# Optimization experiments

Hardware: AMD Instinct MI355X
Metric: run time of the kernel (lower is better)

## Reference

```python
import jax, jax.numpy as jnp
import numpy as np

BLOCK = 64      # sparse block size (power of 2, >= 16)
NB = 128        # number of blocks -> max_seqlen = 8192
LOCAL = 8       # causal local window, in blocks
GLOBAL = 1      # leading global blocks every query attends to
K = LOCAL + GLOBAL
SM_SCALE = 1.0 / np.sqrt(64.0)  # default sm_scale = 1/sqrt(head_dim)


def _build_layout():
    # Fixed-width equivalent of the CSR block layout: for query block i,
    # live key blocks are the GLOBAL leading blocks plus the LOCAL-wide
    # causal window ending at i. Entries outside [0, i] are masked invalid;
    # global entries that fall inside the local window are invalidated to
    # avoid double counting.
    rows = np.arange(NB)[:, None]
    loc = rows - np.arange(LOCAL - 1, -1, -1)[None, :]      # [NB, LOCAL], ascending, ends at i
    glb = np.tile(np.arange(GLOBAL)[None, :], (NB, 1))      # [NB, GLOBAL]
    loc_valid = loc >= 0
    glb_valid = glb < (rows - LOCAL + 1)                    # strictly below local window
    col = np.concatenate([glb, np.maximum(loc, 0)], axis=1)  # [NB, K]
    valid = np.concatenate([glb_valid, loc_valid], axis=1)   # [NB, K]
    return col.astype(np.int32), valid


def setup_inputs() -> dict:
    key = jax.random.key(0)
    kq, kk, kv = jax.random.split(key, 3)
    B, S, H, D = 2, NB * BLOCK, 16, 64
    q = jax.random.normal(kq, (B, S, H, D), jnp.float32)
    k = jax.random.normal(kk, (B, S, H, D), jnp.float32)
    v = jax.random.normal(kv, (B, S, H, D), jnp.float32)
    col, valid = _build_layout()
    return {"q": q, "k": k, "v": v,
            "col_idx": jnp.asarray(col), "col_valid": jnp.asarray(valid)}


def reference(q, k, v, col_idx, col_valid):
    # Block-sparse causal attention. Only key/value blocks listed in
    # col_idx (where col_valid) are touched; token-level causal mask is
    # applied inside the gathered blocks (diagonal blocks get intra-block
    # causal masking, matching the kernel's behavior).
    B, S, H, D = q.shape
    bs = BLOCK
    nb = S // bs
    qb = q.reshape(B, nb, bs, H, D)                       # [B, nb, bs, H, D]
    kb = k.reshape(B, nb, bs, H, D)[:, col_idx]           # [B, nb, K, bs, H, D]
    vb = v.reshape(B, nb, bs, H, D)[:, col_idx]
    scores = jnp.einsum('bimhd,bijnhd->bhimjn', qb, kb) * SM_SCALE  # [B,H,nb,bs,K,bs]
    qpos = jnp.arange(nb)[:, None] * bs + jnp.arange(bs)[None, :]          # [nb, bs]
    kpos = col_idx[:, :, None] * bs + jnp.arange(bs)[None, None, :]        # [nb, K, bs]
    mask = (kpos[:, None, :, :] <= qpos[:, :, None, None]) & col_valid[:, None, :, None]
    neg = jnp.finfo(scores.dtype).min
    scores = jnp.where(mask[None, None], scores, neg)
    shp = scores.shape
    p = jax.nn.softmax(scores.reshape(shp[0], shp[1], shp[2], shp[3], -1), axis=-1).reshape(shp)
    out = jnp.einsum('bhimjn,bijnhd->bimhd', p, vb)       # [B, nb, bs, H, D]
    return out.reshape(B, S, H, D)
```

## Files before the change

kernel.cpp:

```cpp
#include <hip/hip_runtime.h>
#include <hip/hip_bf16.h>

#define NBQ     128
#define NLOCAL  8
#define NH      16
#define NBATCH  2
#define DIM     64
#define SEQ     (NBQ * 64)
#define QK_SCALE 0.1803368801111204f

typedef __attribute__((ext_vector_type(8))) short bf16x8;
typedef __attribute__((ext_vector_type(4))) short short4v;
typedef __attribute__((ext_vector_type(4))) float f32x4;
typedef __attribute__((ext_vector_type(2))) unsigned int u32x2;

__device__ inline short f2b(float x) {
    unsigned int u = __float_as_uint(x);
    return (short)((u + 0x8000u) >> 16);
}
__device__ inline unsigned int pack2(unsigned int lo_rnd, unsigned int hi_rnd) {
    return __builtin_amdgcn_perm(hi_rnd, lo_rnd, 0x07060302u);
}

typedef union { u32x2 u; short4v s; } pk_u;

__global__ __launch_bounds__(256, 4) void sparse_attn_kernel(
    const float* __restrict__ Q, const float* __restrict__ Kg,
    const float* __restrict__ Vg, float* __restrict__ Out)
{
    __shared__ __align__(16) short sK [2][64 * 64];
    __shared__ __align__(16) short sVt[2][64 * 64];

    const int qb  = blockIdx.x >> 5;
    const int bh  = blockIdx.x & 31;
    const int b   = bh >> 4;
    const int h   = bh & 15;
    const int tid  = threadIdx.x;
    const int wave = tid >> 6;
    const int lane = tid & 63;
    const int quad = lane >> 4;
    const int l15  = lane & 15;

    const int sg   = tid >> 4;
    const int t15c = tid & 15;
    const int tok4 = sg << 2;
    const int ft4  = t15c << 2;

    bf16x8 qf[2];
    {
        const int qrow = qb * 64 + wave * 16 + l15;
        const float* qp = Q + (((size_t)(b * SEQ + qrow)) * NH + h) * DIM;
#pragma unroll
        for (int ks = 0; ks < 2; ++ks) {
            const float* p = qp + ks * 32 + quad * 8;
            const f32x4 x0 = *(const f32x4*)(p);
            const f32x4 x1 = *(const f32x4*)(p + 4);
            bf16x8 f;
#pragma unroll
            for (int c = 0; c < 4; ++c) {
                f[c]     = f2b(x0[c] * QK_SCALE);
                f[c + 4] = f2b(x1[c] * QK_SCALE);
            }
            qf[ks] = f;
        }
    }

    float l_part = 0.f;
    f32x4 o_acc[4];
#pragma unroll
    for (int ft = 0; ft < 4; ++ft) o_acc[ft] = (f32x4){0.f, 0.f, 0.f, 0.f};

    const int gsw = l15 & 14;
    const float* kbase = Kg + (size_t)b * (SEQ * NH * DIM);
    const float* vbase = Vg + (size_t)b * (SEQ * NH * DIM);
    const unsigned off0 = (unsigned)((tok4 * NH + h) * DIM + ft4);

    const int kb_lo = (qb - 7 > 0) ? (qb - 7) : 0;
    const int has_g = (qb >= NLOCAL) ? 1 : 0;
    const int niter = (qb - kb_lo + 1) + has_g;

    for (int it = 0; it < niter; ++it) {
        const int kb = (it < has_g) ? 0 : (kb_lo + it - has_g);
        short* sKb = &sK [it & 1][0];
        short* sVb = &sVt[it & 1][0];

        {
            const unsigned koff = ((unsigned)kb << 16) + off0;
            unsigned int kr[4][4], vr[4][4];
#pragma unroll
            for (int i = 0; i < 4; ++i) {
                const f32x4 kx = *(const f32x4*)(kbase + koff + i * (NH * DIM));
                const f32x4 vx = *(const f32x4*)(vbase + koff + i * (NH * DIM));
#pragma unroll
                for (int c = 0; c < 4; ++c) {
                    kr[i][c] = __float_as_uint(kx[c]) + 0x8000u;
                    vr[i][c] = __float_as_uint(vx[c]) + 0x8000u;
                }
            }
#pragma unroll
            for (int i = 0; i < 4; ++i) {
                const int row = tok4 + i;
                const int cp  = t15c ^ (row & 14);
                u32x2 w;
                w.x = pack2(kr[i][0], kr[i][1]);
                w.y = pack2(kr[i][2], kr[i][3]);
                *(u32x2*)&sKb[row * 64 + cp * 4] = w;
            }
#pragma unroll
            for (int c = 0; c < 4; ++c) {
                const int row = ft4 + c;
                const int cp  = sg ^ (row & 14);
                u32x2 w;
                w.x = pack2(vr[0][c], vr[1][c]);
                w.y = pack2(vr[2][c], vr[3][c]);
                *(u32x2*)&sVb[row * 64 + cp * 4] = w;
            }
        }
        __syncthreads();

        f32x4 s[4];
#pragma unroll
        for (int nt = 0; nt < 4; ++nt) {
            const int row = (nt * 16 + l15) * 64;
            const bf16x8 k0 = *(const bf16x8*)&sKb[row + (((2 * quad)     ^ gsw) << 2)];
            const bf16x8 k1 = *(const bf16x8*)&sKb[row + (((8 + 2 * quad) ^ gsw) << 2)];
            f32x4 acc = (f32x4){0.f, 0.f, 0.f, 0.f};
            acc = __builtin_amdgcn_mfma_f32_16x16x32_bf16(k0, qf[0], acc, 0, 0, 0);
            acc = __builtin_amdgcn_mfma_f32_16x16x32_bf16(k1, qf[1], acc, 0, 0, 0);
            s[nt] = acc;
        }

        if (kb == qb) {
            const int qi = wave * 16 + l15;
#pragma unroll
            for (int nt = 0; nt < 4; ++nt)
#pragma unroll
                for (int r = 0; r < 4; ++r) {
                    const int ki = nt * 16 + quad * 4 + r;
                    if (ki > qi) s[nt][r] = -1e30f;
                }
        }

        short4v pb[4];
#pragma unroll
        for (int nt = 0; nt < 4; ++nt) {
            float ps = 0.f;
            unsigned int pr[4];
#pragma unroll
            for (int r = 0; r < 4; ++r) {
                const float p = exp2f(s[nt][r]);
                ps += p;
                pr[r] = __float_as_uint(p) + 0x8000u;
            }
            l_part += ps;
            pk_u pw;
            pw.u.x = pack2(pr[0], pr[1]);
            pw.u.y = pack2(pr[2], pr[3]);
            pb[nt] = pw.s;
        }

#pragma unroll
        for (int ft = 0; ft < 4; ++ft) {
            const int row = (ft * 16 + l15) * 64;
            f32x4 acc = o_acc[ft];
#pragma unroll
            for (int nt = 0; nt < 4; ++nt) {
                const short4v va = *(const short4v*)&sVb[row + (((4 * nt + quad) ^ gsw) << 2)];
                acc = __builtin_amdgcn_mfma_f32_16x16x16bf16_1k(va, pb[nt], acc, 0, 0, 0);
            }
            o_acc[ft] = acc;
        }
    }

    l_part += __shfl_xor(l_part, 16);
    l_part += __shfl_xor(l_part, 32);
    const float inv = 1.0f / l_part;
    const int qrow = qb * 64 + wave * 16 + l15;
    float* op = Out + (((size_t)(b * SEQ + qrow)) * NH + h) * DIM + quad * 4;
#pragma unroll
    for (int ft = 0; ft < 4; ++ft)
        *(f32x4*)(op + ft * 16) = o_acc[ft] * inv;
}

extern "C" void kernel_launch(void* const* d_in, const int* in_sizes, int n_in,
                              void* d_out, int out_size, void* d_ws, size_t ws_size,
                              hipStream_t stream) {
    const float* q = (const float*)d_in[0];
    const float* k = (const float*)d_in[1];
    const float* v = (const float*)d_in[2];
    float* out = (float*)d_out;
    dim3 grid(NBQ * NBATCH * NH);
    sparse_attn_kernel<<<grid, dim3(256), 0, stream>>>(q, k, v, out);
}
```

Measured before the change: 261.0 us.

## Process two query blocks per workgroup to share K/V tile loads

Each workgroup now handles two adjacent query blocks. It loads each K/V block into LDS once and runs the QK and PV MFMAs for whichever query block needs that key block, so overlapping windows no longer reload the same global K/V data. The LDS swizzle patterns for K and transposed V are also changed to new rotation-based layouts. The trade-offs are higher register pressure from duplicated accumulators and half as many workgroups, which lowers parallelism across the device.

```diff
diff --git a/kernel.cpp b/kernel.cpp
--- a/kernel.cpp
+++ b/kernel.cpp
@@ -31,10 +31,11 @@
     __shared__ __align__(16) short sK [2][64 * 64];
     __shared__ __align__(16) short sVt[2][64 * 64];
 
-    const int qb  = blockIdx.x >> 5;
+    const int gq  = blockIdx.x >> 5;
     const int bh  = blockIdx.x & 31;
     const int b   = bh >> 4;
     const int h   = bh & 15;
+    const int qb0 = gq * 2, qb1 = qb0 + 1;
     const int tid  = threadIdx.x;
     const int wave = tid >> 6;
     const int lane = tid & 63;
@@ -46,41 +47,50 @@
     const int tok4 = sg << 2;
     const int ft4  = t15c << 2;
 
-    bf16x8 qf[2];
+    const int swk = l15 & 7;
+    const int swv = ((l15 & 3) << 2) | ((l15 >> 2) & 3);
+
+    bf16x8 qf0[2], qf1[2];
     {
-        const int qrow = qb * 64 + wave * 16 + l15;
-        const float* qp = Q + (((size_t)(b * SEQ + qrow)) * NH + h) * DIM;
+        const int qrow = qb0 * 64 + wave * 16 + l15;
+        const float* qp0 = Q + (((size_t)(b * SEQ + qrow)) * NH + h) * DIM;
+        const float* qp1 = qp0 + (size_t)64 * NH * DIM;
 #pragma unroll
         for (int ks = 0; ks < 2; ++ks) {
-            const float* p = qp + ks * 32 + quad * 8;
-            const f32x4 x0 = *(const f32x4*)(p);
-            const f32x4 x1 = *(const f32x4*)(p + 4);
-            bf16x8 f;
+            const int o = ks * 32 + quad * 8;
+            const f32x4 x0 = *(const f32x4*)(qp0 + o);
+            const f32x4 x1 = *(const f32x4*)(qp0 + o + 4);
+            const f32x4 y0 = *(const f32x4*)(qp1 + o);
+            const f32x4 y1 = *(const f32x4*)(qp1 + o + 4);
+            bf16x8 f, g;
 #pragma unroll
             for (int c = 0; c < 4; ++c) {
                 f[c]     = f2b(x0[c] * QK_SCALE);
                 f[c + 4] = f2b(x1[c] * QK_SCALE);
-            }
-            qf[ks] = f;
+                g[c]     = f2b(y0[c] * QK_SCALE);
+                g[c + 4] = f2b(y1[c] * QK_SCALE);
+            }
+            qf0[ks] = f; qf1[ks] = g;
         }
     }
 
-    float l_part = 0.f;
-    f32x4 o_acc[4];
-#pragma unroll
-    for (int ft = 0; ft < 4; ++ft) o_acc[ft] = (f32x4){0.f, 0.f, 0.f, 0.f};
-
-    const int gsw = l15 & 14;
+    float l0 = 0.f, l1 = 0.f;
+    f32x4 o0[4], o1[4];
+#pragma unroll
+    for (int ft = 0; ft < 4; ++ft) { o0[ft] = (f32x4){0,0,0,0}; o1[ft] = (f32x4){0,0,0,0}; }
+
     const float* kbase = Kg + (size_t)b * (SEQ * NH * DIM);
     const float* vbase = Vg + (size_t)b * (SEQ * NH * DIM);
     const unsigned off0 = (unsigned)((tok4 * NH + h) * DIM + ft4);
 
-    const int kb_lo = (qb - 7 > 0) ? (qb - 7) : 0;
-    const int has_g = (qb >= NLOCAL) ? 1 : 0;
-    const int niter = (qb - kb_lo + 1) + has_g;
+    const int lo    = (qb0 - 7 > 0) ? (qb0 - 7) : 0;
+    const int has_g = (qb0 >= NLOCAL) ? 1 : 0;
+    const int niter = (qb1 - lo + 1) + has_g;
 
     for (int it = 0; it < niter; ++it) {
-        const int kb = (it < has_g) ? 0 : (kb_lo + it - has_g);
+        const int kb = (it < has_g) ? 0 : (lo + it - has_g);
+        const int a0 = (kb == 0 && qb0 >= NLOCAL) || (kb >= qb0 - 7 && kb <= qb0);
+        const int a1 = (kb == 0 && qb1 >= NLOCAL) || (kb >= qb1 - 7 && kb <= qb1);
         short* sKb = &sK [it & 1][0];
         short* sVb = &sVt[it & 1][0];
 
@@ -99,87 +109,117 @@
             }
 #pragma unroll
             for (int i = 0; i < 4; ++i) {
-                const int row = tok4 + i;
-                const int cp  = t15c ^ (row & 14);
+                const int row  = tok4 + i;
+                const int c16p = ((t15c >> 1) + (row & 7)) & 7;
                 u32x2 w;
                 w.x = pack2(kr[i][0], kr[i][1]);
                 w.y = pack2(kr[i][2], kr[i][3]);
-                *(u32x2*)&sKb[row * 64 + cp * 4] = w;
+                *(u32x2*)&sKb[row * 64 + c16p * 8 + (t15c & 1) * 4] = w;
             }
 #pragma unroll
             for (int c = 0; c < 4; ++c) {
                 const int row = ft4 + c;
-                const int cp  = sg ^ (row & 14);
+                const int sig = ((row & 3) << 2) | ((row >> 2) & 3);
+                const int ch8 = (sg + sig) & 15;
                 u32x2 w;
                 w.x = pack2(vr[0][c], vr[1][c]);
                 w.y = pack2(vr[2][c], vr[3][c]);
-                *(u32x2*)&sVb[row * 64 + cp * 4] = w;
+                *(u32x2*)&sVb[row * 64 + ch8 * 4] = w;
             }
         }
         __syncthreads();
 
-        f32x4 s[4];
+        f32x4 s0[4], s1[4];
 #pragma unroll
         for (int nt = 0; nt < 4; ++nt) {
             const int row = (nt * 16 + l15) * 64;
-            const bf16x8 k0 = *(const bf16x8*)&sKb[row + (((2 * quad)     ^ gsw) << 2)];
-            const bf16x8 k1 = *(const bf16x8*)&sKb[row + (((8 + 2 * quad) ^ gsw) << 2)];
-            f32x4 acc = (f32x4){0.f, 0.f, 0.f, 0.f};
-            acc = __builtin_amdgcn_mfma_f32_16x16x32_bf16(k0, qf[0], acc, 0, 0, 0);
-            acc = __builtin_amdgcn_mfma_f32_16x16x32_bf16(k1, qf[1], acc, 0, 0, 0);
-            s[nt] = acc;
-        }
-
-        if (kb == qb) {
+            const bf16x8 k0 = *(const bf16x8*)&sKb[row + (((quad     + swk) & 7) << 3)];
+            const bf16x8 k1 = *(const bf16x8*)&sKb[row + (((4 + quad + swk) & 7) << 3)];
+            if (a0) {
+                f32x4 acc = (f32x4){0,0,0,0};
+                acc = __builtin_amdgcn_mfma_f32_16x16x32_bf16(k0, qf0[0], acc, 0, 0, 0);
+                acc = __builtin_amdgcn_mfma_f32_16x16x32_bf16(k1, qf0[1], acc, 0, 0, 0);
+                s0[nt] = acc;
+            }
+            if (a1) {
+                f32x4 acc = (f32x4){0,0,0,0};
+                acc = __builtin_amdgcn_mfma_f32_16x16x32_bf16(k0, qf1[0], acc, 0, 0, 0);
+                acc = __builtin_amdgcn_mfma_f32_16x16x32_bf16(k1, qf1[1], acc, 0, 0, 0);
+                s1[nt] = acc;
+            }
+        }
+
+        if (kb == qb0) {
             const int qi = wave * 16 + l15;
 #pragma unroll
             for (int nt = 0; nt < 4; ++nt)
 #pragma unroll
+                for (int r = 0; r < 4; ++r)
+                    if (nt * 16 + quad * 4 + r > qi) s0[nt][r] = -1e30f;
+        }
+        if (kb == qb1) {
+            const int qi = wave * 16 + l15;
+#pragma unroll
+            for (int nt = 0; nt < 4; ++nt)
+#pragma unroll
+                for (int r = 0; r < 4; ++r)
+                    if (nt * 16 + quad * 4 + r > qi) s1[nt][r] = -1e30f;
+        }
+
+        short4v pb0[4], pb1[4];
+        if (a0) {
+#pragma unroll
+            for (int nt = 0; nt < 4; ++nt) {
+                float ps = 0.f; unsigned int pr[4];
+#pragma unroll
                 for (int r = 0; r < 4; ++r) {
-                    const int ki = nt * 16 + quad * 4 + r;
-                    if (ki > qi) s[nt][r] = -1e30f;
+                    const float p = exp2f(s0[nt][r]);
+                    ps += p; pr[r] = __float_as_uint(p) + 0x8000u;
                 }
-        }
-
-        short4v pb[4];
-#pragma unroll
-        for (int nt = 0; nt < 4; ++nt) {
-            float ps = 0.f;
-            unsigned int pr[4];
-#pragma unroll
-            for (int r = 0; r < 4; ++r) {
-                const float p = exp2f(s[nt][r]);
-                ps += p;
-                pr[r] = __float_as_uint(p) + 0x8000u;
-            }
-            l_part += ps;
-            pk_u pw;
-            pw.u.x = pack2(pr[0], pr[1]);
-            pw.u.y = pack2(pr[2], pr[3]);
-            pb[nt] = pw.s;
+                l0 += ps;
+                pk_u pw; pw.u.x = pack2(pr[0], pr[1]); pw.u.y = pack2(pr[2], pr[3]);
+                pb0[nt] = pw.s;
+            }
+        }
+        if (a1) {
+#pragma unroll
+            for (int nt = 0; nt < 4; ++nt) {
+                float ps = 0.f; unsigned int pr[4];
+#pragma unroll
+                for (int r = 0; r < 4; ++r) {
+                    const float p = exp2f(s1[nt][r]);
+                    ps += p; pr[r] = __float_as_uint(p) + 0x8000u;
+                }
+                l1 += ps;
+                pk_u pw; pw.u.x = pack2(pr[0], pr[1]); pw.u.y = pack2(pr[2], pr[3]);
+                pb1[nt] = pw.s;
+            }
         }
 
 #pragma unroll
         for (int ft = 0; ft < 4; ++ft) {
             const int row = (ft * 16 + l15) * 64;
-            f32x4 acc = o_acc[ft];
 #pragma unroll
             for (int nt = 0; nt < 4; ++nt) {
-                const short4v va = *(const short4v*)&sVb[row + (((4 * nt + quad) ^ gsw) << 2)];
-                acc = __builtin_amdgcn_mfma_f32_16x16x16bf16_1k(va, pb[nt], acc, 0, 0, 0);
-            }
-            o_acc[ft] = acc;
+                const short4v va = *(const short4v*)&sVb[row + (((nt * 4 + quad + swv) & 15) << 2)];
+                if (a0) o0[ft] = __builtin_amdgcn_mfma_f32_16x16x16bf16_1k(va, pb0[nt], o0[ft], 0, 0, 0);
+                if (a1) o1[ft] = __builtin_amdgcn_mfma_f32_16x16x16bf16_1k(va, pb1[nt], o1[ft], 0, 0, 0);
+            }
         }
     }
 
-    l_part += __shfl_xor(l_part, 16);
-    l_part += __shfl_xor(l_part, 32);
-    const float inv = 1.0f / l_part;
-    const int qrow = qb * 64 + wave * 16 + l15;
-    float* op = Out + (((size_t)(b * SEQ + qrow)) * NH + h) * DIM + quad * 4;
-#pragma unroll
-    for (int ft = 0; ft < 4; ++ft)
-        *(f32x4*)(op + ft * 16) = o_acc[ft] * inv;
+    l0 += __shfl_xor(l0, 16); l0 += __shfl_xor(l0, 32);
+    l1 += __shfl_xor(l1, 16); l1 += __shfl_xor(l1, 32);
+    const float inv0 = 1.0f / l0;
+    const float inv1 = 1.0f / l1;
+    const int qrow = qb0 * 64 + wave * 16 + l15;
+    float* op0 = Out + (((size_t)(b * SEQ + qrow)) * NH + h) * DIM + quad * 4;
+    float* op1 = op0 + (size_t)64 * NH * DIM;
+#pragma unroll
+    for (int ft = 0; ft < 4; ++ft) {
+        *(f32x4*)(op0 + ft * 16) = o0[ft] * inv0;
+        *(f32x4*)(op1 + ft * 16) = o1[ft] * inv1;
+    }
 }
 
 extern "C" void kernel_launch(void* const* d_in, const int* in_sizes, int n_in,
@@ -189,6 +229,6 @@
     const float* k = (const float*)d_in[1];
     const float* v = (const float*)d_in[2];
     float* out = (float*)d_out;
-    dim3 grid(NBQ * NBATCH * NH);
+    dim3 grid((NBQ / 2) * NBATCH * NH);
     sparse_attn_kernel<<<grid, dim3(256), 0, stream>>>(q, k, v, out);
 }
```

Result: slower. 411.1 us (+57.5%).
